# Kernel optimization log

Measured on AMD Instinct MI355X. Metric: run time of the kernel, lower is better.

The kernel has to match this reference:

```python
import jax, jax.numpy as jnp
import numpy as np

NEG_INF = -jnp.inf


def setup_inputs() -> dict:
    key = jax.random.key(0)
    kq, kk, kv = jax.random.split(key, 3)
    B, L, H, E = 2, 2048, 16, 64
    queries = jax.random.normal(kq, (B, L, H, E), dtype=jnp.float32)
    keys = jax.random.normal(kk, (B, L, H, E), dtype=jnp.float32)
    values = jax.random.normal(kv, (B, L, H, E), dtype=jnp.float32)
    return {"queries": queries, "keys": keys, "values": values}


def reference(queries, keys, values):
    B, L, H, E = queries.shape
    scale = 1.0 / jnp.sqrt(jnp.asarray(E, dtype=queries.dtype))
    # scores: [B, H, L, S]
    scores = jnp.einsum("blhe,bshe->bhls", queries, keys)
    # causal mask: True above the diagonal -> masked out
    causal = jnp.triu(jnp.ones((L, L), dtype=bool), k=1)
    scores = jnp.where(causal[None, None, :, :], NEG_INF, scores)
    A = jax.nn.softmax(scale * scores, axis=-1)
    # output: [B, L, H, D]
    V = jnp.einsum("bhls,bshd->blhd", A, values)
    return V
```

## Files before the change

### kernel.cpp

```cpp
#include <hip/hip_runtime.h>


using f32x4  = __attribute__((ext_vector_type(4))) float;
using bf16x8 = __attribute__((ext_vector_type(8))) short;
using u32x2  = __attribute__((ext_vector_type(2))) unsigned int;
using u32x4  = __attribute__((ext_vector_type(4))) unsigned int;

constexpr int L = 2048;
constexpr int H = 16;
constexpr int E = 64;
constexpr int KVBLK = 64;
constexpr float QSC = 0.125f * 1.44269504088896f;
constexpr float KNB = 24.0f;
constexpr float THR = 8.0f;

#if defined(__has_builtin)
#if __has_builtin(__builtin_amdgcn_exp2f)
#define HAVE_EXP2 1
#endif
#endif
__device__ __forceinline__ float fexp2(float x) {
#ifdef HAVE_EXP2
    return __builtin_amdgcn_exp2f(x);
#else
    float r;
    asm("v_exp_f32 %0, %1" : "=v"(r) : "v"(x));
    return r;
#endif
}

__device__ __forceinline__ unsigned cvt_pk(float lo, float hi) {
    unsigned r;
    asm("v_cvt_pk_bf16_f32 %0, %1, %2" : "=v"(r) : "v"(lo), "v"(hi));
    return r;
}
__device__ __forceinline__ void pl16(unsigned& a, unsigned& b) {
    asm("v_permlane16_swap_b32 %0, %1" : "+v"(a), "+v"(b));
}
__device__ __forceinline__ void pl32(unsigned& a, unsigned& b) {
    asm("v_permlane32_swap_b32 %0, %1" : "+v"(a), "+v"(b));
}
__device__ __forceinline__ unsigned opaque_copy(unsigned a) {
    unsigned b;
    asm("v_mov_b32 %0, %1" : "=v"(b) : "v"(a));
    return b;
}
__device__ __forceinline__ float gmax4(float x) {
    unsigned a = __float_as_uint(x), b = opaque_copy(a);
    pl16(a, b);
    float m = fmaxf(__uint_as_float(a), __uint_as_float(b));
    unsigned c = __float_as_uint(m), d = opaque_copy(c);
    pl32(c, d);
    return fmaxf(__uint_as_float(c), __uint_as_float(d));
}
__device__ __forceinline__ float gsum4(float x) {
    unsigned a = __float_as_uint(x), b = opaque_copy(a);
    pl16(a, b);
    float s = __uint_as_float(a) + __uint_as_float(b);
    unsigned c = __float_as_uint(s), d = opaque_copy(c);
    pl32(c, d);
    return __uint_as_float(c) + __uint_as_float(d);
}
__device__ __forceinline__ int swz(int row, int bcol) {
    return (row * 128 + bcol) ^ ((row & 7) << 4);
}
__device__ __forceinline__ int swzV(int row, int bcol) {
    return (row * 128 + bcol) ^ ((((row & 7) ^ (row >> 3)) & 7) << 4);
}
__device__ __forceinline__ void gload16(const short* g, short* l) {
    __builtin_amdgcn_global_load_lds(
        (const __attribute__((address_space(1))) void*)g,
        (__attribute__((address_space(3))) void*)l, 16, 0, 0);
}

__global__ __launch_bounds__(256)
void prep_kernel(const float* __restrict__ K, const float* __restrict__ V,
                 short* __restrict__ Kb, short* __restrict__ Vb)
{
    __shared__ float Vt[64][65];
    const int bx  = blockIdx.x;
    const int t   = bx & 31;
    const int bh  = bx >> 5;
    const int tid = threadIdx.x;
    const size_t bhoff = (size_t)(bh >> 4) * L * (H * E) + (size_t)(bh & 15) * E;
    const size_t tileo = (size_t)(bh * 32 + t) * 4096;

    #pragma unroll
    for (int g = 0; g < 2; ++g) {
        const int c  = g * 256 + tid;
        const int r  = c >> 3;
        const int e0 = (c & 7) * 8;
        const float* kp = K + bhoff + (size_t)(t * 64 + r) * 1024 + e0;
        f32x4 k0 = *(const f32x4*)kp, k1 = *(const f32x4*)(kp + 4);
        u32x4 kt;
        kt[0] = cvt_pk(k0[0], k0[1]); kt[1] = cvt_pk(k0[2], k0[3]);
        kt[2] = cvt_pk(k1[0], k1[1]); kt[3] = cvt_pk(k1[2], k1[3]);
        *(u32x4*)(Kb + tileo + r * 64 + (((e0 >> 3) ^ (r & 7)) * 8)) = kt;
        const float* vp = V + bhoff + (size_t)(t * 64 + r) * 1024 + e0;
        f32x4 v0 = *(const f32x4*)vp, v1 = *(const f32x4*)(vp + 4);
        #pragma unroll
        for (int k2 = 0; k2 < 4; ++k2) { Vt[r][e0 + k2] = v0[k2]; Vt[r][e0 + 4 + k2] = v1[k2]; }
    }
    __syncthreads();
    #pragma unroll
    for (int g = 0; g < 2; ++g) {
        const int c  = g * 256 + tid;
        const int d  = c >> 3;
        const int jp = c & 7;
        const int F  = ((d & 7) ^ (d >> 3)) & 7;
        const int col0 = 8 * (jp ^ F);
        float vals[8];
        #pragma unroll
        for (int i = 0; i < 8; ++i) {
            const int col = col0 + i;
            const int s = 16 * ((col >> 3) & 3) + 8 * (col >> 5) + (col & 7);
            vals[i] = Vt[s][d];
        }
        u32x4 vt;
        vt[0] = cvt_pk(vals[0], vals[1]); vt[1] = cvt_pk(vals[2], vals[3]);
        vt[2] = cvt_pk(vals[4], vals[5]); vt[3] = cvt_pk(vals[6], vals[7]);
        *(u32x4*)(Vb + tileo + d * 64 + jp * 8) = vt;
    }
}

__global__ __launch_bounds__(256, 2)
void fattn_main(const float* __restrict__ Q,
                const short* __restrict__ Kb,
                const short* __restrict__ Vb,
                float* __restrict__ O)
{
    __shared__ short Kl[2][4096];
    __shared__ short Vl[2][4096];

    const int bx  = blockIdx.x;
    const int xcd = bx & 7;
    const int j   = bx >> 3;
    const int bh  = (j & 3) * 8 + xcd;
    const int pa  = j >> 2;
    const int tid = threadIdx.x;
    const int w    = tid >> 6;
    const int lane = tid & 63;
    const int l16  = lane & 15;
    const int lhi  = lane >> 4;

    const size_t bhoff  = (size_t)(bh >> 4) * L * (H * E) + (size_t)(bh & 15) * E;
    const int rs_ = H * E;
    const size_t kvbase = (size_t)bh * 32 * 4096;

    const int wboff = w * 2048 + lane * 16;
    const int wlds  = w * 2048;

    auto stage = [&](int t, int buf) {
        const char* kt = (const char*)(Kb + kvbase) + (size_t)t * 8192 + wboff;
        const char* vt = (const char*)(Vb + kvbase) + (size_t)t * 8192 + wboff;
        gload16((const short*)kt,          Kl[buf] + wlds / 2);
        gload16((const short*)(kt + 1024), Kl[buf] + (wlds + 1024) / 2);
        gload16((const short*)vt,          Vl[buf] + wlds / 2);
        gload16((const short*)(vt + 1024), Vl[buf] + (wlds + 1024) / 2);
    };

    const int iq0 = 31 - pa, iq1 = pa;
    const int total0 = iq0 + 1;
    const int total  = total0 + iq1 + 1;

    bf16x8 qf[2];
    float m_fix = 0.0f;
    int qg = 0;
    auto load_q = [&](int iq) {
        qg = iq * 64 + w * 16 + l16;
        float qn2 = 0.0f;
        const float* qp = Q + bhoff + (size_t)qg * rs_ + lhi * 8;
        #pragma unroll
        for (int kf = 0; kf < 2; ++kf) {
            f32x4 xv = *(const f32x4*)(qp + kf * 32);
            f32x4 yv = *(const f32x4*)(qp + kf * 32 + 4);
            #pragma unroll
            for (int k2 = 0; k2 < 4; ++k2) {
                qn2 += xv[k2] * xv[k2];
                qn2 += yv[k2] * yv[k2];
            }
            union { u32x4 u; bf16x8 hh; } r;
            r.u[0] = cvt_pk(xv[0] * QSC, xv[1] * QSC);
            r.u[1] = cvt_pk(xv[2] * QSC, xv[3] * QSC);
            r.u[2] = cvt_pk(yv[0] * QSC, yv[1] * QSC);
            r.u[3] = cvt_pk(yv[2] * QSC, yv[3] * QSC);
            qf[kf] = r.hh;
        }
        m_fix = sqrtf(gsum4(qn2)) * (KNB * QSC);
    };

    f32x4 oacc[4];
    f32x4 rsv;
    auto reset_acc = [&]() {
        #pragma unroll
        for (int dt = 0; dt < 4; ++dt) oacc[dt] = (f32x4){0.f, 0.f, 0.f, 0.f};
        rsv = (f32x4){0.f, 0.f, 0.f, 0.f};
    };
    auto store_o = [&]() {
        const float lsum = gsum4((rsv[0] + rsv[1]) + (rsv[2] + rsv[3]));
        const float inv = 1.0f / lsum;
        float* op = O + bhoff + (size_t)qg * rs_;
        #pragma unroll
        for (int dt = 0; dt < 4; ++dt) {
            f32x4 o = oacc[dt];
            o[0] *= inv; o[1] *= inv; o[2] *= inv; o[3] *= inv;
            *(f32x4*)(op + dt * 16 + lhi * 4) = o;
        }
    };

    stage(0, 0);
    load_q(iq0);
    reset_acc();

    __builtin_amdgcn_sched_barrier(0);
    asm volatile("s_waitcnt vmcnt(0)" ::: "memory");
    __builtin_amdgcn_s_barrier();
    __builtin_amdgcn_sched_barrier(0);

    for (int i = 0; i < total; ++i) {
        const int ts = (i < total0) ? i : (i - total0);
        if (i == total0) {
            store_o();
            load_q(iq1);
            reset_acc();
        }

        if (i + 1 < total) {
            const int nts = (i + 1 < total0) ? (i + 1) : (i + 1 - total0);
            stage(nts, (i + 1) & 1);
        }

        const char* Kbl = (const char*)Kl[i & 1];
        const char* Vbl = (const char*)Vl[i & 1];

        f32x4 p[4];
        #pragma unroll
        for (int st = 0; st < 4; ++st) p[st] = (f32x4){0.f, 0.f, 0.f, 0.f};
        #pragma unroll
        for (int st = 0; st < 4; ++st) {
            #pragma unroll
            for (int kf = 0; kf < 2; ++kf) {
                bf16x8 af = *(const bf16x8*)(Kbl + swz(st * 16 + l16, (lhi * 8 + kf * 32) * 2));
                p[st] = __builtin_amdgcn_mfma_f32_16x16x32_bf16(af, qf[kf], p[st], 0, 0, 0);
            }
        }

        if (i == total0 - 1 || i == total - 1) {
            #pragma unroll
            for (int st = 0; st < 4; ++st)
                #pragma unroll
                for (int r = 0; r < 4; ++r) {
                    const int kg = ts * KVBLK + st * 16 + lhi * 4 + r;
                    if (kg > qg) p[st][r] = -INFINITY;
                }
        }

        #pragma unroll
        for (int st = 0; st < 4; ++st)
            #pragma unroll
            for (int r = 0; r < 4; ++r) {
                const float e = fexp2(p[st][r] - m_fix);
                p[st][r] = e;
                rsv[r] += e;
            }

        unsigned wp[4][2];
        #pragma unroll
        for (int st = 0; st < 4; ++st) {
            wp[st][0] = cvt_pk(p[st][0], p[st][1]);
            wp[st][1] = cvt_pk(p[st][2], p[st][3]);
        }
        #pragma unroll
        for (int hh = 0; hh < 2; ++hh) {
            pl16(wp[0][hh], wp[1][hh]);
            pl16(wp[2][hh], wp[3][hh]);
            pl32(wp[0][hh], wp[2][hh]);
            pl32(wp[1][hh], wp[3][hh]);
        }
        union { u32x4 u; bf16x8 v; } pb0, pb1;
        pb0.u[0] = wp[0][0]; pb0.u[1] = wp[0][1];
        pb0.u[2] = wp[1][0]; pb0.u[3] = wp[1][1];
        pb1.u[0] = wp[2][0]; pb1.u[1] = wp[2][1];
        pb1.u[2] = wp[3][0]; pb1.u[3] = wp[3][1];

        #pragma unroll
        for (int dt = 0; dt < 4; ++dt) {
            bf16x8 vf0 = *(const bf16x8*)(Vbl + swzV(dt * 16 + l16, (lhi * 8) * 2));
            oacc[dt] = __builtin_amdgcn_mfma_f32_16x16x32_bf16(vf0, pb0.v, oacc[dt], 0, 0, 0);
            bf16x8 vf1 = *(const bf16x8*)(Vbl + swzV(dt * 16 + l16, (lhi * 8 + 32) * 2));
            oacc[dt] = __builtin_amdgcn_mfma_f32_16x16x32_bf16(vf1, pb1.v, oacc[dt], 0, 0, 0);
        }

        if (i + 1 < total) {
            __builtin_amdgcn_sched_barrier(0);
            asm volatile("s_waitcnt vmcnt(0)" ::: "memory");
            __builtin_amdgcn_s_barrier();
            __builtin_amdgcn_sched_barrier(0);
        }
    }

    store_o();
}

__global__ __launch_bounds__(256, 4)
void fattn_fb(const float* __restrict__ Q,
              const float* __restrict__ K,
              const float* __restrict__ V,
              float* __restrict__ O)
{
    __shared__ short Kl[2][KVBLK * 64];
    __shared__ short Vl[2][64 * KVBLK];

    const int bx  = blockIdx.x;
    const int xcd = bx & 7;
    const int j   = bx >> 3;
    const int bh  = (j & 3) * 8 + xcd;
    const int v_  = j >> 2;
    const int q2  = v_ >> 3, x_ = v_ & 7;
    const int iq  = (q2 & 1) ? (31 - (q2 >> 1) - 2 * x_) : (2 * x_ + (q2 >> 1));
    const int tid = threadIdx.x;
    const int w    = tid >> 6;
    const int lane = tid & 63;
    const int l16  = lane & 15;
    const int lhi  = lane >> 4;

    const size_t bhoff = (size_t)(bh >> 4) * L * (H * E) + (size_t)(bh & 15) * E;
    const int rs_ = H * E;
    const int sv0 = (tid >> 4) * 4;
    const int d0  = (tid & 15) * 4;
    const int kc  = ((sv0 >> 3) & 1) * 32 + (sv0 >> 4) * 8 + (sv0 & 7);

    f32x4 ka[2][2];
    f32x4 va[4];
    auto issue_loads = [&](int t) {
        const int sb = t * KVBLK;
        #pragma unroll
        for (int g = 0; g < 2; ++g) {
            const int c = g * 256 + tid;
            const int s = c >> 3;
            const int e0 = (c & 7) * 8;
            const f32x4* kp = (const f32x4*)(K + bhoff + (size_t)(sb + s) * rs_ + e0);
            ka[g][0] = kp[0];
            ka[g][1] = kp[1];
        }
        #pragma unroll
        for (int jj = 0; jj < 4; ++jj)
            va[jj] = *(const f32x4*)(V + bhoff + (size_t)(sb + sv0 + jj) * rs_ + d0);
    };
    auto write_lds = [&](int bufi) {
        short* Kb = Kl[bufi];
        short* Vb = Vl[bufi];
        #pragma unroll
        for (int g = 0; g < 2; ++g) {
            const int c = g * 256 + tid;
            const int s = c >> 3;
            const int e0 = (c & 7) * 8;
            u32x4 kt;
            kt[0] = cvt_pk(ka[g][0][0], ka[g][0][1]);
            kt[1] = cvt_pk(ka[g][0][2], ka[g][0][3]);
            kt[2] = cvt_pk(ka[g][1][0], ka[g][1][1]);
            kt[3] = cvt_pk(ka[g][1][2], ka[g][1][3]);
            *(u32x4*)((char*)Kb + swz(s, e0 * 2)) = kt;
        }
        #pragma unroll
        for (int dd = 0; dd < 4; ++dd) {
            u32x2 vt;
            vt[0] = cvt_pk(va[0][dd], va[1][dd]);
            vt[1] = cvt_pk(va[2][dd], va[3][dd]);
            *(u32x2*)((char*)Vb + swzV(d0 + dd, kc * 2)) = vt;
        }
    };

    const int qg = iq * 64 + w * 16 + l16;
    bf16x8 qf[2];
    {
        const float* qp = Q + bhoff + (size_t)qg * rs_ + lhi * 8;
        #pragma unroll
        for (int kf = 0; kf < 2; ++kf) {
            f32x4 xv = *(const f32x4*)(qp + kf * 32);
            f32x4 yv = *(const f32x4*)(qp + kf * 32 + 4);
            union { u32x4 u; bf16x8 hh; } r;
            r.u[0] = cvt_pk(xv[0] * QSC, xv[1] * QSC);
            r.u[1] = cvt_pk(xv[2] * QSC, xv[3] * QSC);
            r.u[2] = cvt_pk(yv[0] * QSC, yv[1] * QSC);
            r.u[3] = cvt_pk(yv[2] * QSC, yv[3] * QSC);
            qf[kf] = r.hh;
        }
    }

    float m_run = -INFINITY, lsum = 0.0f;
    f32x4 oacc[4];
    #pragma unroll
    for (int dt = 0; dt < 4; ++dt) oacc[dt] = (f32x4){0.f, 0.f, 0.f, 0.f};

    const int total = iq + 1;
    issue_loads(0);
    write_lds(0);
    if (total > 1) issue_loads(1);
    __syncthreads();

    for (int i = 0; i < total; ++i) {
        const char* Kbl = (const char*)Kl[i & 1];
        const char* Vbl = (const char*)Vl[i & 1];
        f32x4 p[4];
        #pragma unroll
        for (int st = 0; st < 4; ++st) p[st] = (f32x4){0.f, 0.f, 0.f, 0.f};
        #pragma unroll
        for (int st = 0; st < 4; ++st) {
            #pragma unroll
            for (int kf = 0; kf < 2; ++kf) {
                bf16x8 af = *(const bf16x8*)(Kbl + swz(st * 16 + l16, (lhi * 8 + kf * 32) * 2));
                p[st] = __builtin_amdgcn_mfma_f32_16x16x32_bf16(af, qf[kf], p[st], 0, 0, 0);
            }
        }
        if (i == total - 1) {
            #pragma unroll
            for (int st = 0; st < 4; ++st)
                #pragma unroll
                for (int r = 0; r < 4; ++r) {
                    const int kg = i * KVBLK + st * 16 + lhi * 4 + r;
                    if (kg > qg) p[st][r] = -INFINITY;
                }
        }
        if (i + 1 < total) write_lds((i + 1) & 1);
        if (i + 2 < total) issue_loads(i + 2);

        f32x4 mv = p[0];
        #pragma unroll
        for (int st = 1; st < 4; ++st)
            #pragma unroll
            for (int r = 0; r < 4; ++r) mv[r] = fmaxf(mv[r], p[st][r]);
        float mx = fmaxf(fmaxf(mv[0], mv[1]), fmaxf(mv[2], mv[3]));
        mx = gmax4(mx);
        if (!__all(mx <= m_run + THR)) {
            const float mn = fmaxf(m_run, mx);
            const float corr = fexp2(m_run - mn);
            lsum *= corr;
            #pragma unroll
            for (int dt = 0; dt < 4; ++dt)
                #pragma unroll
                for (int r = 0; r < 4; ++r) oacc[dt][r] *= corr;
            m_run = mn;
        }
        f32x4 rsv = (f32x4){0.f, 0.f, 0.f, 0.f};
        #pragma unroll
        for (int st = 0; st < 4; ++st)
            #pragma unroll
            for (int r = 0; r < 4; ++r) {
                const float e = fexp2(p[st][r] - m_run);
                p[st][r] = e;
                rsv[r] += e;
            }
        lsum += gsum4((rsv[0] + rsv[1]) + (rsv[2] + rsv[3]));

        unsigned wp[4][2];
        #pragma unroll
        for (int st = 0; st < 4; ++st) {
            wp[st][0] = cvt_pk(p[st][0], p[st][1]);
            wp[st][1] = cvt_pk(p[st][2], p[st][3]);
        }
        #pragma unroll
        for (int hh = 0; hh < 2; ++hh) {
            pl16(wp[0][hh], wp[1][hh]);
            pl16(wp[2][hh], wp[3][hh]);
            pl32(wp[0][hh], wp[2][hh]);
            pl32(wp[1][hh], wp[3][hh]);
        }
        union { u32x4 u; bf16x8 v; } pb0, pb1;
        pb0.u[0] = wp[0][0]; pb0.u[1] = wp[0][1];
        pb0.u[2] = wp[1][0]; pb0.u[3] = wp[1][1];
        pb1.u[0] = wp[2][0]; pb1.u[1] = wp[2][1];
        pb1.u[2] = wp[3][0]; pb1.u[3] = wp[3][1];

        #pragma unroll
        for (int dt = 0; dt < 4; ++dt) {
            bf16x8 vf0 = *(const bf16x8*)(Vbl + swzV(dt * 16 + l16, (lhi * 8) * 2));
            oacc[dt] = __builtin_amdgcn_mfma_f32_16x16x32_bf16(vf0, pb0.v, oacc[dt], 0, 0, 0);
            bf16x8 vf1 = *(const bf16x8*)(Vbl + swzV(dt * 16 + l16, (lhi * 8 + 32) * 2));
            oacc[dt] = __builtin_amdgcn_mfma_f32_16x16x32_bf16(vf1, pb1.v, oacc[dt], 0, 0, 0);
        }
        if (i + 1 < total) __syncthreads();
    }

    const float inv = 1.0f / lsum;
    float* op = O + bhoff + (size_t)qg * rs_;
    #pragma unroll
    for (int dt = 0; dt < 4; ++dt) {
        f32x4 o = oacc[dt];
        o[0] *= inv; o[1] *= inv; o[2] *= inv; o[3] *= inv;
        *(f32x4*)(op + dt * 16 + lhi * 4) = o;
    }
}

extern "C" void kernel_launch(void* const* d_in, const int* in_sizes, int n_in,
                              void* d_out, int out_size, void* d_ws, size_t ws_size,
                              hipStream_t stream) {
    const float* Q = (const float*)d_in[0];
    const float* K = (const float*)d_in[1];
    const float* V = (const float*)d_in[2];
    float* O = (float*)d_out;
    const size_t kb_elems = (size_t)32 * 32 * 4096;
    if (ws_size >= 2 * kb_elems * sizeof(short)) {
        short* Kb = (short*)d_ws;
        short* Vb = Kb + kb_elems;
        prep_kernel<<<1024, 256, 0, stream>>>(K, V, Kb, Vb);
        fattn_main<<<512, 256, 0, stream>>>(Q, Kb, Vb, O);
    } else {
        fattn_fb<<<1024, 256, 0, stream>>>(Q, K, V, O);
    }
}
```

Measured before the change: 49.64 us.

## Add split-KV causal attention kernel with 128-row query blocks and reduce pass

```diff
diff --git a/kernel.cpp b/kernel.cpp
--- a/kernel.cpp
+++ b/kernel.cpp
@@ -13,6 +13,7 @@
 constexpr float QSC = 0.125f * 1.44269504088896f;
 constexpr float KNB = 24.0f;
 constexpr float THR = 8.0f;
+constexpr int NCH = 38 * 32;
 
 #if defined(__has_builtin)
 #if __has_builtin(__builtin_amdgcn_exp2f)
@@ -123,6 +124,249 @@
     }
 }
 
+__global__ __launch_bounds__(256, 4)
+void fattn_splitk(const float* __restrict__ Q,
+                  const short* __restrict__ Kb,
+                  const short* __restrict__ Vb,
+                  float* __restrict__ Op,
+                  float* __restrict__ Lp)
+{
+    __shared__ short Kl[2][4096];
+    __shared__ short Vl[2][4096];
+
+    const int S_[17] = {0,1,2,3,4,6,8,10,12,14,17,20,23,26,30,34,38};
+
+    const int bx  = blockIdx.x;
+    const int xcd = bx & 7;
+    const int q_  = bx >> 3;
+    const int bhl = q_ / 38;
+    const int c   = 37 - (q_ % 38);
+    const int bh  = bhl * 8 + xcd;
+    int u = 0;
+    #pragma unroll
+    for (int x = 1; x < 16; ++x) if (c >= S_[x]) u = x;
+    const int j  = c - S_[u];
+    const int T  = 2 * u + 2;
+    const int k  = S_[u + 1] - S_[u];
+    const int t0 = (j * T) / k;
+    const int t1 = ((j + 1) * T) / k;
+    const int chunk = bh * 38 + c;
+
+    const int tid = threadIdx.x;
+    const int w    = tid >> 6;
+    const int lane = tid & 63;
+    const int l16  = lane & 15;
+    const int lhi  = lane >> 4;
+
+    const size_t bhoff  = (size_t)(bh >> 4) * L * (H * E) + (size_t)(bh & 15) * E;
+    const int rs_ = H * E;
+    const size_t kvbase = (size_t)bh * 32 * 4096;
+
+    const int wboff = w * 2048 + lane * 16;
+    const int wlds  = w * 2048;
+
+    auto stage = [&](int t, int buf) {
+        const char* kt = (const char*)(Kb + kvbase) + (size_t)t * 8192 + wboff;
+        const char* vt = (const char*)(Vb + kvbase) + (size_t)t * 8192 + wboff;
+        gload16((const short*)kt,          Kl[buf] + wlds / 2);
+        gload16((const short*)(kt + 1024), Kl[buf] + (wlds + 1024) / 2);
+        gload16((const short*)vt,          Vl[buf] + wlds / 2);
+        gload16((const short*)(vt + 1024), Vl[buf] + (wlds + 1024) / 2);
+    };
+
+    const int qg0 = u * 128 + w * 32 + l16;
+    const int qg1 = qg0 + 16;
+    stage(t0, 0);
+
+    bf16x8 qfA[2], qfB[2];
+    float m_fixA, m_fixB;
+    {
+        float qn2 = 0.0f;
+        const float* qp = Q + bhoff + (size_t)qg0 * rs_ + lhi * 8;
+        #pragma unroll
+        for (int kf = 0; kf < 2; ++kf) {
+            f32x4 xv = *(const f32x4*)(qp + kf * 32);
+            f32x4 yv = *(const f32x4*)(qp + kf * 32 + 4);
+            #pragma unroll
+            for (int k2 = 0; k2 < 4; ++k2) { qn2 += xv[k2]*xv[k2]; qn2 += yv[k2]*yv[k2]; }
+            union { u32x4 u4; bf16x8 hh; } r;
+            r.u4[0] = cvt_pk(xv[0] * QSC, xv[1] * QSC);
+            r.u4[1] = cvt_pk(xv[2] * QSC, xv[3] * QSC);
+            r.u4[2] = cvt_pk(yv[0] * QSC, yv[1] * QSC);
+            r.u4[3] = cvt_pk(yv[2] * QSC, yv[3] * QSC);
+            qfA[kf] = r.hh;
+        }
+        m_fixA = sqrtf(gsum4(qn2)) * (KNB * QSC);
+    }
+    {
+        float qn2 = 0.0f;
+        const float* qp = Q + bhoff + (size_t)qg1 * rs_ + lhi * 8;
+        #pragma unroll
+        for (int kf = 0; kf < 2; ++kf) {
+            f32x4 xv = *(const f32x4*)(qp + kf * 32);
+            f32x4 yv = *(const f32x4*)(qp + kf * 32 + 4);
+            #pragma unroll
+            for (int k2 = 0; k2 < 4; ++k2) { qn2 += xv[k2]*xv[k2]; qn2 += yv[k2]*yv[k2]; }
+            union { u32x4 u4; bf16x8 hh; } r;
+            r.u4[0] = cvt_pk(xv[0] * QSC, xv[1] * QSC);
+            r.u4[1] = cvt_pk(xv[2] * QSC, xv[3] * QSC);
+            r.u4[2] = cvt_pk(yv[0] * QSC, yv[1] * QSC);
+            r.u4[3] = cvt_pk(yv[2] * QSC, yv[3] * QSC);
+            qfB[kf] = r.hh;
+        }
+        m_fixB = sqrtf(gsum4(qn2)) * (KNB * QSC);
+    }
+
+    f32x4 oaccA[4], oaccB[4];
+    #pragma unroll
+    for (int dt = 0; dt < 4; ++dt) {
+        oaccA[dt] = (f32x4){0.f, 0.f, 0.f, 0.f};
+        oaccB[dt] = (f32x4){0.f, 0.f, 0.f, 0.f};
+    }
+    f32x4 rsvA = (f32x4){0.f, 0.f, 0.f, 0.f};
+    f32x4 rsvB = (f32x4){0.f, 0.f, 0.f, 0.f};
+
+    __builtin_amdgcn_sched_barrier(0);
+    asm volatile("s_waitcnt vmcnt(0)" ::: "memory");
+    __builtin_amdgcn_s_barrier();
+    __builtin_amdgcn_sched_barrier(0);
+
+    for (int t = t0; t < t1; ++t) {
+        const int it = t - t0;
+        if (t + 1 < t1) stage(t + 1, (it + 1) & 1);
+
+        const char* Kbl = (const char*)Kl[it & 1];
+        const char* Vbl = (const char*)Vl[it & 1];
+
+        f32x4 pA[4], pB[4];
+        #pragma unroll
+        for (int st = 0; st < 4; ++st) {
+            bf16x8 af0 = *(const bf16x8*)(Kbl + swz(st * 16 + l16, (lhi * 8) * 2));
+            bf16x8 af1 = *(const bf16x8*)(Kbl + swz(st * 16 + l16, (lhi * 8 + 32) * 2));
+            pA[st] = __builtin_amdgcn_mfma_f32_16x16x32_bf16(
+                        af0, qfA[0], (f32x4){0.f, 0.f, 0.f, 0.f}, 0, 0, 0);
+            pB[st] = __builtin_amdgcn_mfma_f32_16x16x32_bf16(
+                        af0, qfB[0], (f32x4){0.f, 0.f, 0.f, 0.f}, 0, 0, 0);
+            pA[st] = __builtin_amdgcn_mfma_f32_16x16x32_bf16(af1, qfA[1], pA[st], 0, 0, 0);
+            pB[st] = __builtin_amdgcn_mfma_f32_16x16x32_bf16(af1, qfB[1], pB[st], 0, 0, 0);
+        }
+
+        if (t >= 2 * u) {
+            #pragma unroll
+            for (int st = 0; st < 4; ++st)
+                #pragma unroll
+                for (int r = 0; r < 4; ++r) {
+                    const int kg = t * KVBLK + st * 16 + lhi * 4 + r;
+                    if (kg > qg0) pA[st][r] = -INFINITY;
+                    if (kg > qg1) pB[st][r] = -INFINITY;
+                }
+        }
+
+        #pragma unroll
+        for (int st = 0; st < 4; ++st)
+            #pragma unroll
+            for (int r = 0; r < 4; ++r) {
+                const float eA = fexp2(pA[st][r] - m_fixA);
+                const float eB = fexp2(pB[st][r] - m_fixB);
+                pA[st][r] = eA; rsvA[r] += eA;
+                pB[st][r] = eB; rsvB[r] += eB;
+            }
+
+        unsigned wpA[4][2], wpB[4][2];
+        #pragma unroll
+        for (int st = 0; st < 4; ++st) {
+            wpA[st][0] = cvt_pk(pA[st][0], pA[st][1]);
+            wpA[st][1] = cvt_pk(pA[st][2], pA[st][3]);
+            wpB[st][0] = cvt_pk(pB[st][0], pB[st][1]);
+            wpB[st][1] = cvt_pk(pB[st][2], pB[st][3]);
+        }
+        #pragma unroll
+        for (int hh = 0; hh < 2; ++hh) {
+            pl16(wpA[0][hh], wpA[1][hh]);
+            pl16(wpA[2][hh], wpA[3][hh]);
+            pl32(wpA[0][hh], wpA[2][hh]);
+            pl32(wpA[1][hh], wpA[3][hh]);
+            pl16(wpB[0][hh], wpB[1][hh]);
+            pl16(wpB[2][hh], wpB[3][hh]);
+            pl32(wpB[0][hh], wpB[2][hh]);
+            pl32(wpB[1][hh], wpB[3][hh]);
+        }
+        union { u32x4 u4; bf16x8 v; } pbA0, pbA1, pbB0, pbB1;
+        pbA0.u4[0] = wpA[0][0]; pbA0.u4[1] = wpA[0][1];
+        pbA0.u4[2] = wpA[1][0]; pbA0.u4[3] = wpA[1][1];
+        pbA1.u4[0] = wpA[2][0]; pbA1.u4[1] = wpA[2][1];
+        pbA1.u4[2] = wpA[3][0]; pbA1.u4[3] = wpA[3][1];
+        pbB0.u4[0] = wpB[0][0]; pbB0.u4[1] = wpB[0][1];
+        pbB0.u4[2] = wpB[1][0]; pbB0.u4[3] = wpB[1][1];
+        pbB1.u4[0] = wpB[2][0]; pbB1.u4[1] = wpB[2][1];
+        pbB1.u4[2] = wpB[3][0]; pbB1.u4[3] = wpB[3][1];
+
+        #pragma unroll
+        for (int dt = 0; dt < 4; ++dt) {
+            bf16x8 vf0 = *(const bf16x8*)(Vbl + swzV(dt * 16 + l16, (lhi * 8) * 2));
+            bf16x8 vf1 = *(const bf16x8*)(Vbl + swzV(dt * 16 + l16, (lhi * 8 + 32) * 2));
+            oaccA[dt] = __builtin_amdgcn_mfma_f32_16x16x32_bf16(vf0, pbA0.v, oaccA[dt], 0, 0, 0);
+            oaccB[dt] = __builtin_amdgcn_mfma_f32_16x16x32_bf16(vf0, pbB0.v, oaccB[dt], 0, 0, 0);
+            oaccA[dt] = __builtin_amdgcn_mfma_f32_16x16x32_bf16(vf1, pbA1.v, oaccA[dt], 0, 0, 0);
+            oaccB[dt] = __builtin_amdgcn_mfma_f32_16x16x32_bf16(vf1, pbB1.v, oaccB[dt], 0, 0, 0);
+        }
+
+        if (t + 1 < t1) {
+            __builtin_amdgcn_sched_barrier(0);
+            asm volatile("s_waitcnt vmcnt(0)" ::: "memory");
+            __builtin_amdgcn_s_barrier();
+            __builtin_amdgcn_sched_barrier(0);
+        }
+    }
+
+    const float lsumA = gsum4((rsvA[0] + rsvA[1]) + (rsvA[2] + rsvA[3]));
+    const float lsumB = gsum4((rsvB[0] + rsvB[1]) + (rsvB[2] + rsvB[3]));
+    const int rlA = w * 32 + l16;
+    const int rlB = rlA + 16;
+    float* opA = Op + ((size_t)chunk * 128 + rlA) * 64;
+    float* opB = Op + ((size_t)chunk * 128 + rlB) * 64;
+    #pragma unroll
+    for (int dt = 0; dt < 4; ++dt) {
+        *(f32x4*)(opA + dt * 16 + lhi * 4) = oaccA[dt];
+        *(f32x4*)(opB + dt * 16 + lhi * 4) = oaccB[dt];
+    }
+    if (lhi == 0) {
+        Lp[chunk * 128 + rlA] = lsumA;
+        Lp[chunk * 128 + rlB] = lsumB;
+    }
+}
+
+__global__ __launch_bounds__(256)
+void reduce_kernel(const float* __restrict__ Op,
+                   const float* __restrict__ Lp,
+                   float* __restrict__ O)
+{
+    const int S_[17] = {0,1,2,3,4,6,8,10,12,14,17,20,23,26,30,34,38};
+    const int bx = blockIdx.x;
+    const int bh = bx >> 4;
+    const int u  = bx & 15;
+    const int cb = bh * 38 + S_[u];
+    const int k  = S_[u + 1] - S_[u];
+    const int tid = threadIdx.x;
+    const int row = tid >> 1;
+    const int d0  = (tid & 1) * 32;
+
+    float ls = 0.0f;
+    for (int j = 0; j < k; ++j) ls += Lp[(size_t)(cb + j) * 128 + row];
+    const float inv = 1.0f / ls;
+
+    const size_t bhoff = (size_t)(bh >> 4) * L * (H * E) + (size_t)(bh & 15) * E;
+    float* o = O + bhoff + (size_t)(u * 128 + row) * (H * E);
+    #pragma unroll
+    for (int dd = 0; dd < 8; ++dd) {
+        f32x4 a = (f32x4){0.f, 0.f, 0.f, 0.f};
+        for (int j = 0; j < k; ++j)
+            a += *(const f32x4*)(Op + ((size_t)(cb + j) * 128 + row) * 64 + d0 + dd * 4);
+        a[0] *= inv; a[1] *= inv; a[2] *= inv; a[3] *= inv;
+        *(f32x4*)(o + d0 + dd * 4) = a;
+    }
+}
+
 __global__ __launch_bounds__(256, 2)
 void fattn_main(const float* __restrict__ Q,
                 const short* __restrict__ Kb,
@@ -175,15 +419,12 @@
             f32x4 xv = *(const f32x4*)(qp + kf * 32);
             f32x4 yv = *(const f32x4*)(qp + kf * 32 + 4);
             #pragma unroll
-            for (int k2 = 0; k2 < 4; ++k2) {
-                qn2 += xv[k2] * xv[k2];
-                qn2 += yv[k2] * yv[k2];
-            }
-            union { u32x4 u; bf16x8 hh; } r;
-            r.u[0] = cvt_pk(xv[0] * QSC, xv[1] * QSC);
-            r.u[1] = cvt_pk(xv[2] * QSC, xv[3] * QSC);
-            r.u[2] = cvt_pk(yv[0] * QSC, yv[1] * QSC);
-            r.u[3] = cvt_pk(yv[2] * QSC, yv[3] * QSC);
+            for (int k2 = 0; k2 < 4; ++k2) { qn2 += xv[k2]*xv[k2]; qn2 += yv[k2]*yv[k2]; }
+            union { u32x4 u4; bf16x8 hh; } r;
+            r.u4[0] = cvt_pk(xv[0] * QSC, xv[1] * QSC);
+            r.u4[1] = cvt_pk(xv[2] * QSC, xv[3] * QSC);
+            r.u4[2] = cvt_pk(yv[0] * QSC, yv[1] * QSC);
+            r.u4[3] = cvt_pk(yv[2] * QSC, yv[3] * QSC);
             qf[kf] = r.hh;
         }
         m_fix = sqrtf(gsum4(qn2)) * (KNB * QSC);
@@ -224,7 +465,6 @@
             load_q(iq1);
             reset_acc();
         }
-
         if (i + 1 < total) {
             const int nts = (i + 1 < total0) ? (i + 1) : (i + 1 - total0);
             stage(nts, (i + 1) & 1);
@@ -277,11 +517,11 @@
             pl32(wp[0][hh], wp[2][hh]);
             pl32(wp[1][hh], wp[3][hh]);
         }
-        union { u32x4 u; bf16x8 v; } pb0, pb1;
-        pb0.u[0] = wp[0][0]; pb0.u[1] = wp[0][1];
-        pb0.u[2] = wp[1][0]; pb0.u[3] = wp[1][1];
-        pb1.u[0] = wp[2][0]; pb1.u[1] = wp[2][1];
-        pb1.u[2] = wp[3][0]; pb1.u[3] = wp[3][1];
+        union { u32x4 u4; bf16x8 v; } pb0, pb1;
+        pb0.u4[0] = wp[0][0]; pb0.u4[1] = wp[0][1];
+        pb0.u4[2] = wp[1][0]; pb0.u4[3] = wp[1][1];
+        pb1.u4[0] = wp[2][0]; pb1.u4[1] = wp[2][1];
+        pb1.u4[2] = wp[3][0]; pb1.u4[3] = wp[3][1];
 
         #pragma unroll
         for (int dt = 0; dt < 4; ++dt) {
@@ -379,11 +619,11 @@
         for (int kf = 0; kf < 2; ++kf) {
             f32x4 xv = *(const f32x4*)(qp + kf * 32);
             f32x4 yv = *(const f32x4*)(qp + kf * 32 + 4);
-            union { u32x4 u; bf16x8 hh; } r;
-            r.u[0] = cvt_pk(xv[0] * QSC, xv[1] * QSC);
-            r.u[1] = cvt_pk(xv[2] * QSC, xv[3] * QSC);
-            r.u[2] = cvt_pk(yv[0] * QSC, yv[1] * QSC);
-            r.u[3] = cvt_pk(yv[2] * QSC, yv[3] * QSC);
+            union { u32x4 u4; bf16x8 hh; } r;
+            r.u4[0] = cvt_pk(xv[0] * QSC, xv[1] * QSC);
+            r.u4[1] = cvt_pk(xv[2] * QSC, xv[3] * QSC);
+            r.u4[2] = cvt_pk(yv[0] * QSC, yv[1] * QSC);
+            r.u4[3] = cvt_pk(yv[2] * QSC, yv[3] * QSC);
             qf[kf] = r.hh;
         }
     }
@@ -466,11 +706,11 @@
             pl32(wp[0][hh], wp[2][hh]);
             pl32(wp[1][hh], wp[3][hh]);
         }
-        union { u32x4 u; bf16x8 v; } pb0, pb1;
-        pb0.u[0] = wp[0][0]; pb0.u[1] = wp[0][1];
-        pb0.u[2] = wp[1][0]; pb0.u[3] = wp[1][1];
-        pb1.u[0] = wp[2][0]; pb1.u[1] = wp[2][1];
-        pb1.u[2] = wp[3][0]; pb1.u[3] = wp[3][1];
+        union { u32x4 u4; bf16x8 v; } pb0, pb1;
+        pb0.u4[0] = wp[0][0]; pb0.u4[1] = wp[0][1];
+        pb0.u4[2] = wp[1][0]; pb0.u4[3] = wp[1][1];
+        pb1.u4[0] = wp[2][0]; pb1.u4[1] = wp[2][1];
+        pb1.u4[2] = wp[3][0]; pb1.u4[3] = wp[3][1];
 
         #pragma unroll
         for (int dt = 0; dt < 4; ++dt) {
@@ -499,8 +739,19 @@
     const float* K = (const float*)d_in[1];
     const float* V = (const float*)d_in[2];
     float* O = (float*)d_out;
-    const size_t kb_elems = (size_t)32 * 32 * 4096;
-    if (ws_size >= 2 * kb_elems * sizeof(short)) {
+    const size_t kb_elems    = (size_t)32 * 32 * 4096;
+    const size_t tiles_bytes = 2 * kb_elems * sizeof(short);
+    const size_t op_bytes    = (size_t)NCH * 128 * 64 * 4;
+    const size_t lp_bytes    = (size_t)NCH * 128 * 4;
+    if (ws_size >= tiles_bytes + op_bytes + lp_bytes) {
+        short* Kb = (short*)d_ws;
+        short* Vb = Kb + kb_elems;
+        float* Op = (float*)((char*)d_ws + tiles_bytes);
+        float* Lp = (float*)((char*)d_ws + tiles_bytes + op_bytes);
+        prep_kernel<<<1024, 256, 0, stream>>>(K, V, Kb, Vb);
+        fattn_splitk<<<NCH, 256, 0, stream>>>(Q, Kb, Vb, Op, Lp);
+        reduce_kernel<<<512, 256, 0, stream>>>(Op, Lp, O);
+    } else if (ws_size >= tiles_bytes) {
         short* Kb = (short*)d_ws;
         short* Vb = Kb + kb_elems;
         prep_kernel<<<1024, 256, 0, stream>>>(K, V, Kb, Vb);
```

Measured after the change: 112.0 us. +125.7%, slower.
